# Kernel optimization log

Hardware: AMD Instinct MI355X
Metric: run time of the kernel (lower is better)

Reference implementation:

```python
import jax, jax.numpy as jnp
import numpy as np

B, N, D, H, L = 2, 2048, 128, 8, 3
V = 32          # NUM_ATOM_TYPES (assumed)
DH = D // H
SCALE = 1.0 / (DH ** 0.5)
NEG = -1e9      # stands in for -inf in the additive attention mask
EPS = 1e-5


def _ln(x, g, b):
    m = x.mean(-1, keepdims=True)
    v = ((x - m) ** 2).mean(-1, keepdims=True)
    return (x - m) / jnp.sqrt(v + EPS) * g + b


def setup_inputs() -> dict:
    key = jax.random.key(0)
    ks = jax.random.split(key, 24)
    nrm = lambda k, shape, std=0.02: jax.random.normal(k, shape, jnp.float32) * std
    atom_embed = nrm(ks[0], (V, D)).at[0].set(0.0)  # padding_idx = 0
    cons_embed = nrm(ks[1], (1, 1, D))
    in_w = nrm(ks[2], (D, D)); in_b = jnp.zeros((D,), jnp.float32)
    qkv_w = nrm(ks[3], (L, 3 * D, D)); qkv_b = jnp.zeros((L, 3 * D), jnp.float32)
    out_w = nrm(ks[4], (L, D, D)); out_b = jnp.zeros((L, D), jnp.float32)
    ln1_g = jnp.ones((L, D), jnp.float32); ln1_b = jnp.zeros((L, D), jnp.float32)
    ln2_g = jnp.ones((L, D), jnp.float32); ln2_b = jnp.zeros((L, D), jnp.float32)
    ff1_w = nrm(ks[5], (L, 4 * D, D)); ff1_b = jnp.zeros((L, 4 * D), jnp.float32)
    ff2_w = nrm(ks[6], (L, D, 4 * D)); ff2_b = jnp.zeros((L, D), jnp.float32)
    struct_bias = nrm(ks[7], (L,), 0.5)  # scalar per layer (init 0 in torch; randomized to exercise the path)
    head_ln_g = jnp.ones((D,), jnp.float32); head_ln_b = jnp.zeros((D,), jnp.float32)
    head_w = nrm(ks[8], (1, D)); head_b = jnp.zeros((1,), jnp.float32)
    is_atom = jax.random.bernoulli(ks[9], 0.5, (B, N))
    atom_id = jax.random.randint(ks[10], (B, N), 0, V)
    mask = jax.random.bernoulli(ks[11], 0.9, (B, N))
    adjacency = (jax.random.uniform(ks[12], (B, N, N)) < 0.002).astype(jnp.float32)
    adjacency = jnp.maximum(adjacency, jnp.eye(N, dtype=jnp.float32)[None])  # self-loops
    root_idx = jax.random.randint(ks[13], (B,), 0, N)
    return dict(atom_embed=atom_embed, cons_embed=cons_embed, in_w=in_w, in_b=in_b,
                qkv_w=qkv_w, qkv_b=qkv_b, out_w=out_w, out_b=out_b,
                ln1_g=ln1_g, ln1_b=ln1_b, ln2_g=ln2_g, ln2_b=ln2_b,
                ff1_w=ff1_w, ff1_b=ff1_b, ff2_w=ff2_w, ff2_b=ff2_b,
                struct_bias=struct_bias, head_ln_g=head_ln_g, head_ln_b=head_ln_b,
                head_w=head_w, head_b=head_b, adjacency=adjacency,
                is_atom=is_atom, atom_id=atom_id, mask=mask, root_idx=root_idx)


def reference(atom_embed, cons_embed, in_w, in_b, qkv_w, qkv_b, out_w, out_b,
              ln1_g, ln1_b, ln2_g, ln2_b, ff1_w, ff1_b, ff2_w, ff2_b,
              struct_bias, head_ln_g, head_ln_b, head_w, head_b,
              adjacency, is_atom, atom_id, mask, root_idx):
    # node embeddings
    ae = atom_embed[jnp.clip(atom_id, 0, V - 1)]                     # [B,N,D]
    h = jnp.where(is_atom[..., None], ae, jnp.broadcast_to(cons_embed, (B, N, D)))
    h = h @ in_w.T + in_b
    # additive attention mask: valid pairs OK; invalid query rows attend only to self
    pair_ok = mask[:, :, None] & mask[:, None, :]
    eye = jnp.eye(N, dtype=bool)[None]
    ok = pair_ok | ((~mask)[:, :, None] & eye)
    am = jnp.where(ok, 0.0, NEG).astype(jnp.float32)                 # [B,N,N]
    for i in range(L):
        x = _ln(h, ln1_g[i], ln1_b[i])
        qkv = (x @ qkv_w[i].T + qkv_b[i]).reshape(B, N, 3, H, DH)
        q, k, v = (jnp.transpose(qkv[:, :, j], (0, 2, 1, 3)) for j in range(3))  # [B,H,N,DH]
        scores = jnp.einsum('bhqd,bhkd->bhqk', q, k) * SCALE \
                 + struct_bias[i] * adjacency[:, None] + am[:, None]
        attn = jax.nn.softmax(scores, axis=-1)
        o = jnp.einsum('bhqk,bhkd->bhqd', attn, v)
        o = jnp.transpose(o, (0, 2, 1, 3)).reshape(B, N, D)
        h = h + (o @ out_w[i].T + out_b[i])
        x2 = _ln(h, ln2_g[i], ln2_b[i])
        f = jax.nn.gelu(x2 @ ff1_w[i].T + ff1_b[i], approximate=False)
        h = h + (f @ ff2_w[i].T + ff2_b[i])
    pooled = h[jnp.arange(B), root_idx]                              # [B,D]
    p = _ln(pooled, head_ln_g, head_ln_b)
    return (p @ head_w.T + head_b)[:, 0]                             # [B]
```

## Files before the change

kernel.cpp:

```cpp
#include <hip/hip_runtime.h>
#include <cmath>

#define NB 2
#define NN 2048
#define ND 128
#define NH 8
#define NL 3
#define NV 32
#define NDH 16
#define LN_EPS 1e-5f
#define QSCALE 0.36067376022224085f

typedef __bf16 bf8_t __attribute__((ext_vector_type(8)));
typedef __bf16 bf4_t __attribute__((ext_vector_type(4)));
typedef float f4x __attribute__((ext_vector_type(4)));
typedef float f16x __attribute__((ext_vector_type(16)));

struct CastArgs {
  const float* s[5];
  __bf16* d[5];
  int startblk[5];
};
__global__ __launch_bounds__(256) void prep_kernel(
    CastArgs a, const float* __restrict__ adj, unsigned long long* __restrict__ abits,
    const int* __restrict__ mask, unsigned long long* __restrict__ mbits) {
  int blk = blockIdx.x;
  int lane = threadIdx.x & 63;
  if (blk < 592) {
    int seg = 0;
#pragma unroll
    for (int i = 1; i < 5; i++) seg += (blk >= a.startblk[i]) ? 1 : 0;
    int i4 = (blk - a.startblk[seg]) * 256 + threadIdx.x;
    float4 v = ((const float4*)a.s[seg])[i4];
    bf4_t p = {(__bf16)v.x, (__bf16)v.y, (__bf16)v.z, (__bf16)v.w};
    ((bf4_t*)a.d[seg])[i4] = p;
  } else if (blk < 592 + 8192) {
    int g = ((blk - 592) * 4 + (threadIdx.x >> 6)) * 4;
    const float* p = adj + (size_t)g * 64 + lane;
    unsigned long long w0 = __ballot(p[0] != 0.0f);
    unsigned long long w1 = __ballot(p[64] != 0.0f);
    unsigned long long w2 = __ballot(p[128] != 0.0f);
    unsigned long long w3 = __ballot(p[192] != 0.0f);
    if (lane == 0) {
      abits[g] = w0; abits[g + 1] = w1; abits[g + 2] = w2; abits[g + 3] = w3;
    }
  } else {
    int g = (blk - 8784) * 4 + (threadIdx.x >> 6);
    int v = mask[g * 64 + lane];
    unsigned long long bal = __ballot(v != 0);
    if (lane == 0) mbits[g] = bal;
  }
}

__global__ __launch_bounds__(512) void fused0_kernel(
    const float* __restrict__ atom_embed, const float* __restrict__ cons_embed,
    const int* __restrict__ is_atom, const int* __restrict__ atom_id,
    const __bf16* __restrict__ W1, const float* __restrict__ b1,
    float* __restrict__ Hout,
    const float* __restrict__ lng, const float* __restrict__ lnb,
    const __bf16* __restrict__ W2, const float* __restrict__ b2,
    __bf16* __restrict__ Qb, __bf16* __restrict__ Kb, __bf16* __restrict__ Vt) {
  __shared__ __bf16 Xs[16][136];
  __shared__ __bf16 Ws[128][136];
  __shared__ float Hs[16][132];
  __shared__ __bf16 X2[16][136];
  int m0 = blockIdx.x * 16;
  int g = blockIdx.y;
  int t = threadIdx.x;
  int lane = t & 63, w = t >> 6;
  int l15 = lane & 15, quad = lane >> 4;
  const int NC2 = (g == 0) ? 2 : 1;
  const int T = 1 + NC2;

  {
    int r = t >> 5, c = t & 31;
    int row = m0 + r;
    int id = atom_id[row];
    id = id < 0 ? 0 : (id > NV - 1 ? NV - 1 : id);
    const float* src = is_atom[row] ? (atom_embed + (size_t)id * ND) : cons_embed;
    float4 v = *(const float4*)&src[c * 4];
    bf4_t p = {(__bf16)v.x, (__bf16)v.y, (__bf16)v.z, (__bf16)v.w};
    *(bf4_t*)&Xs[r][c * 4] = p;
  }

  bf8_t wreg[4];
  auto issue = [&](int i) {
    const __bf16* base;
    int rowoff;
    if (i == 0) { base = W1; rowoff = 0; }
    else {
      int nc = (g == 0) ? (i - 1) : 2;
      base = W2; rowoff = nc * 128;
    }
#pragma unroll
    for (int jj = 0; jj < 4; jj++) {
      int c = t + jj * 512;
      wreg[jj] = *(const bf8_t*)&base[(size_t)(rowoff + (c >> 4)) * 128 + (c & 15) * 8];
    }
  };
  issue(0);

  for (int i = 0; i < T; i++) {
    if (i) __syncthreads();
#pragma unroll
    for (int jj = 0; jj < 4; jj++) {
      int c = t + jj * 512;
      *(bf8_t*)&Ws[c >> 4][(c & 15) * 8] = wreg[jj];
    }
    __syncthreads();
    if (i + 1 < T) issue(i + 1);
    if (i == 0) {
      f4x a1 = {0.f, 0.f, 0.f, 0.f};
#pragma unroll
      for (int kk = 0; kk < 4; kk++) {
        bf8_t a = *(const bf8_t*)&Xs[l15][kk * 32 + quad * 8];
        bf8_t b = *(const bf8_t*)&Ws[w * 16 + l15][kk * 32 + quad * 8];
        a1 = __builtin_amdgcn_mfma_f32_16x16x32_bf16(a, b, a1, 0, 0, 0);
      }
      int n = w * 16 + l15;
      float bv = b1[n];
#pragma unroll
      for (int r = 0; r < 4; r++) {
        int m = quad * 4 + r;
        float v = a1[r] + bv;
        if (g == 0) Hout[(size_t)(m0 + m) * ND + n] = v;
        Hs[m][n] = v;
      }
      __syncthreads();
      {
        int r = t >> 5, c = t & 31;
        float4 v = *(const float4*)&Hs[r][c * 4];
        float s1 = v.x + v.y + v.z + v.w;
        float s2 = v.x * v.x + v.y * v.y + v.z * v.z + v.w * v.w;
#pragma unroll
        for (int m = 16; m >= 1; m >>= 1) {
          s1 += __shfl_xor(s1, m, 64);
          s2 += __shfl_xor(s2, m, 64);
        }
        float mean = s1 * (1.0f / ND);
        float var = s2 * (1.0f / ND) - mean * mean;
        float rstd = rsqrtf(var + LN_EPS);
        float4 gg = *(const float4*)&lng[c * 4];
        float4 bb = *(const float4*)&lnb[c * 4];
        bf4_t p;
        p[0] = (__bf16)((v.x - mean) * rstd * gg.x + bb.x);
        p[1] = (__bf16)((v.y - mean) * rstd * gg.y + bb.y);
        p[2] = (__bf16)((v.z - mean) * rstd * gg.z + bb.z);
        p[3] = (__bf16)((v.w - mean) * rstd * gg.w + bb.w);
        *(bf4_t*)&X2[r][c * 4] = p;
      }
    } else {
      int nc = (g == 0) ? (i - 1) : 2;
      f4x a2 = {0.f, 0.f, 0.f, 0.f};
#pragma unroll
      for (int kk = 0; kk < 4; kk++) {
        bf8_t a = *(const bf8_t*)&X2[l15][kk * 32 + quad * 8];
        bf8_t b = *(const bf8_t*)&Ws[w * 16 + l15][kk * 32 + quad * 8];
        a2 = __builtin_amdgcn_mfma_f32_16x16x32_bf16(a, b, a2, 0, 0, 0);
      }
      int n = nc * 128 + w * 16 + l15;
      float bv = b2[n];
#pragma unroll
      for (int r = 0; r < 4; r++) {
        int m = m0 + quad * 4 + r;
        float v = a2[r] + bv;
        if (n < ND) Qb[(size_t)m * ND + n] = (__bf16)(v * QSCALE);
        else if (n < 2 * ND) Kb[(size_t)m * ND + n - ND] = (__bf16)v;
        else {
          int c2 = n - 2 * ND, hh = c2 >> 4, d0 = c2 & 15;
          int bb2 = m >> 11, nn = m & 2047;
          Vt[((size_t)((bb2 * NH + hh) * NDH + d0)) * NN + nn] = (__bf16)v;
        }
      }
    }
  }
}

template <int LAST>
__global__ __launch_bounds__(512) void layer_kernel(
    const __bf16* __restrict__ Ob,
    const __bf16* __restrict__ Wout, const float* __restrict__ bout,
    const float* __restrict__ Hin, float* __restrict__ Hout,
    const float* __restrict__ ln2g, const float* __restrict__ ln2b,
    const __bf16* __restrict__ Wff1, const float* __restrict__ bff1,
    const __bf16* __restrict__ Wff2, const float* __restrict__ bff2,
    const float* __restrict__ ln1g, const float* __restrict__ ln1b,
    const __bf16* __restrict__ Wqkv, const float* __restrict__ bqkv,
    __bf16* __restrict__ Qb, __bf16* __restrict__ Kb, __bf16* __restrict__ Vt,
    const int* __restrict__ root_idx, const float* __restrict__ hg,
    const float* __restrict__ hbt, const float* __restrict__ hwp,
    const float* __restrict__ hbp, float* __restrict__ outp) {
  __shared__ __bf16 Xs[16][136];
  __shared__ __bf16 Ws[128][136];
  __shared__ float Hs[16][132];
  __shared__ __bf16 X2[16][136];
  __shared__ __bf16 Fs[16][520];
  int m0 = blockIdx.x * 16;
  int g = blockIdx.y;
  int t = threadIdx.x;
  int lane = t & 63, w = t >> 6;
  int l15 = lane & 15, quad = lane >> 4;
  const int NQ = LAST ? 0 : (g == 0 ? 2 : 1);
  const int T = 9 + NQ;

  {
    int r = t >> 5, c = t & 31;
    *(bf4_t*)&Xs[r][c * 4] = *(const bf4_t*)&Ob[(size_t)(m0 + r) * ND + c * 4];
  }

  bf8_t wreg[4];
  auto issue = [&](int i) {
    const __bf16* base;
    int stride, rowoff, coloff;
    if (i == 0)     { base = Wout; stride = 128; rowoff = 0;             coloff = 0; }
    else if (i < 5) { base = Wff1; stride = 128; rowoff = (i - 1) * 128; coloff = 0; }
    else if (i < 9) { base = Wff2; stride = 512; rowoff = 0;             coloff = (i - 5) * 128; }
    else            { int nc = (g == 0) ? (i - 9) : 2;
                      base = Wqkv; stride = 128; rowoff = nc * 128;      coloff = 0; }
#pragma unroll
    for (int jj = 0; jj < 4; jj++) {
      int c = t + jj * 512;
      wreg[jj] = *(const bf8_t*)&base[(size_t)(rowoff + (c >> 4)) * stride + coloff + (c & 15) * 8];
    }
  };
  issue(0);

  auto do_ln = [&](const float* g_, const float* b_) {
    int r = t >> 5, c = t & 31;
    float4 v = *(const float4*)&Hs[r][c * 4];
    float s1 = v.x + v.y + v.z + v.w;
    float s2 = v.x * v.x + v.y * v.y + v.z * v.z + v.w * v.w;
#pragma unroll
    for (int m = 16; m >= 1; m >>= 1) {
      s1 += __shfl_xor(s1, m, 64);
      s2 += __shfl_xor(s2, m, 64);
    }
    float mean = s1 * (1.0f / ND);
    float var = s2 * (1.0f / ND) - mean * mean;
    float rstd = rsqrtf(var + LN_EPS);
    float4 gg = *(const float4*)&g_[c * 4];
    float4 bb = *(const float4*)&b_[c * 4];
    bf4_t p;
    p[0] = (__bf16)((v.x - mean) * rstd * gg.x + bb.x);
    p[1] = (__bf16)((v.y - mean) * rstd * gg.y + bb.y);
    p[2] = (__bf16)((v.z - mean) * rstd * gg.z + bb.z);
    p[3] = (__bf16)((v.w - mean) * rstd * gg.w + bb.w);
    *(bf4_t*)&X2[r][c * 4] = p;
  };

  f4x acc2 = {0.f, 0.f, 0.f, 0.f};
  for (int i = 0; i < T; i++) {
    if (i) __syncthreads();
#pragma unroll
    for (int jj = 0; jj < 4; jj++) {
      int c = t + jj * 512;
      *(bf8_t*)&Ws[c >> 4][(c & 15) * 8] = wreg[jj];
    }
    __syncthreads();
    if (i + 1 < T) issue(i + 1);
    if (i == 0) {
      f4x a1 = {0.f, 0.f, 0.f, 0.f};
#pragma unroll
      for (int kk = 0; kk < 4; kk++) {
        bf8_t a = *(const bf8_t*)&Xs[l15][kk * 32 + quad * 8];
        bf8_t b = *(const bf8_t*)&Ws[w * 16 + l15][kk * 32 + quad * 8];
        a1 = __builtin_amdgcn_mfma_f32_16x16x32_bf16(a, b, a1, 0, 0, 0);
      }
      int n = w * 16 + l15;
      float bv = bout[n];
#pragma unroll
      for (int r = 0; r < 4; r++) {
        int m = quad * 4 + r;
        Hs[m][n] = a1[r] + bv + Hin[(size_t)(m0 + m) * ND + n];
      }
      __syncthreads();
      do_ln(ln2g, ln2b);
    } else if (i < 5) {
      int c = i - 1;
      f4x a1 = {0.f, 0.f, 0.f, 0.f};
#pragma unroll
      for (int kk = 0; kk < 4; kk++) {
        bf8_t a = *(const bf8_t*)&X2[l15][kk * 32 + quad * 8];
        bf8_t b = *(const bf8_t*)&Ws[w * 16 + l15][kk * 32 + quad * 8];
        a1 = __builtin_amdgcn_mfma_f32_16x16x32_bf16(a, b, a1, 0, 0, 0);
      }
      int n = w * 16 + l15;
      float bv = bff1[c * 128 + n];
#pragma unroll
      for (int r = 0; r < 4; r++) {
        float v = a1[r] + bv;
        v = 0.5f * v * (1.0f + erff(v * 0.70710678118f));
        Fs[quad * 4 + r][c * 128 + n] = (__bf16)v;
      }
    } else if (i < 9) {
      int j = i - 5;
#pragma unroll
      for (int kk = 0; kk < 4; kk++) {
        bf8_t a = *(const bf8_t*)&Fs[l15][j * 128 + kk * 32 + quad * 8];
        bf8_t b = *(const bf8_t*)&Ws[w * 16 + l15][kk * 32 + quad * 8];
        acc2 = __builtin_amdgcn_mfma_f32_16x16x32_bf16(a, b, acc2, 0, 0, 0);
      }
      if (j == 3) {
        int n = w * 16 + l15;
        float bv = bff2[n];
#pragma unroll
        for (int r = 0; r < 4; r++) {
          int m = quad * 4 + r;
          float v = acc2[r] + bv + Hs[m][n];
          Hs[m][n] = v;
          if (g == 0) Hout[(size_t)(m0 + m) * ND + n] = v;
        }
        __syncthreads();
        if constexpr (!LAST) do_ln(ln1g, ln1b);
      }
    } else {
      int nc = (g == 0) ? (i - 9) : 2;
      f4x a2 = {0.f, 0.f, 0.f, 0.f};
#pragma unroll
      for (int kk = 0; kk < 4; kk++) {
        bf8_t a = *(const bf8_t*)&X2[l15][kk * 32 + quad * 8];
        bf8_t b = *(const bf8_t*)&Ws[w * 16 + l15][kk * 32 + quad * 8];
        a2 = __builtin_amdgcn_mfma_f32_16x16x32_bf16(a, b, a2, 0, 0, 0);
      }
      int n = nc * 128 + w * 16 + l15;
      float bv = bqkv[n];
#pragma unroll
      for (int r = 0; r < 4; r++) {
        int m = m0 + quad * 4 + r;
        float v = a2[r] + bv;
        if (n < ND) Qb[(size_t)m * ND + n] = (__bf16)(v * QSCALE);
        else if (n < 2 * ND) Kb[(size_t)m * ND + n - ND] = (__bf16)v;
        else {
          int c2 = n - 2 * ND, hh = c2 >> 4, d0 = c2 & 15;
          int bb2 = m >> 11, nn = m & 2047;
          Vt[((size_t)((bb2 * NH + hh) * NDH + d0)) * NN + nn] = (__bf16)v;
        }
      }
    }
  }

  if constexpr (LAST) {
    if (w < NB) {
      int rt = root_idx[w];
      int rglob = w * NN + rt;
      if (rglob >= m0 && rglob < m0 + 16) {
        int r = rglob - m0;
        float v0 = Hs[r][2 * lane], v1 = Hs[r][2 * lane + 1];
        float s1 = v0 + v1, s2 = v0 * v0 + v1 * v1;
#pragma unroll
        for (int m = 32; m >= 1; m >>= 1) {
          s1 += __shfl_xor(s1, m, 64);
          s2 += __shfl_xor(s2, m, 64);
        }
        float mean = s1 * (1.0f / ND);
        float var = s2 * (1.0f / ND) - mean * mean;
        float rstd = rsqrtf(var + LN_EPS);
        float p0 = (v0 - mean) * rstd * hg[2 * lane] + hbt[2 * lane];
        float p1 = (v1 - mean) * rstd * hg[2 * lane + 1] + hbt[2 * lane + 1];
        float part = p0 * hwp[2 * lane] + p1 * hwp[2 * lane + 1];
#pragma unroll
        for (int m = 32; m >= 1; m >>= 1) part += __shfl_xor(part, m, 64);
        if (lane == 0) outp[w] = part + hbp[0];
      }
    }
  }
}

__global__ __launch_bounds__(512) void attn_kernel(
    const __bf16* __restrict__ Qb, const __bf16* __restrict__ Kb,
    const __bf16* __restrict__ Vt, const unsigned int* __restrict__ adjbits,
    const unsigned int* __restrict__ maskbits, const int* __restrict__ mask,
    const float* __restrict__ sbias, int layer, __bf16* __restrict__ o) {
  int b = blockIdx.z, hh = blockIdx.y, q0 = blockIdx.x * 32;
  int wave = threadIdx.x >> 6;
  int lane = threadIdx.x & 63;
  int l31 = lane & 31, hi = lane >> 5;
  int l15 = lane & 15, quad = lane >> 4;
  float esb = __expf(sbias[layer]);
  const int bN = b * NN;
  const int kw0 = wave * 256;

  __shared__ __bf16 Pbuf[8][32][40];
  __shared__ float Ored[8][32][17];
  __shared__ float Lred[8][32];

  bf8_t Qf = *(const bf8_t*)(Qb + (size_t)(bN + q0 + l31) * ND + hh * NDH + hi * 8);

  int q = q0 + l31;
  int mq = mask[bN + q];
  const unsigned int* adjp = adjbits + (size_t)(bN + q) * (NN / 32) + (kw0 >> 5);
  const unsigned int* mbp = maskbits + (bN + kw0) / 32;
  const __bf16* kp = Kb + (size_t)(bN + kw0 + l31) * ND + hh * NDH + hi * 8;
  const __bf16* vp = Vt + (size_t)((b * NH + hh) * NDH + l15) * NN + kw0 + quad * 8;

  int dq = q - kw0;
  int tsel = dq >> 5;
  unsigned int selfw = 1u << (dq & 31);
  int sh4 = hi * 4;

  f4x Olo = {0.f, 0.f, 0.f, 0.f}, Ohi = {0.f, 0.f, 0.f, 0.f};
  float ls = 0.f;

  bf8_t Kf = *(const bf8_t*)kp;
  bf8_t Vf = *(const bf8_t*)vp;
  unsigned int aw = adjp[0];
  unsigned int mkw = mbp[0];

  for (int t = 0; t < 8; t++) {
    bf8_t Kn = Kf, Vn = Vf;
    unsigned int awn = aw, mkn = mkw;
    if (t < 7) {
      kp += 32 * ND;
      Kn = *(const bf8_t*)kp;
      Vn = *(const bf8_t*)(vp + (t + 1) * 32);
      awn = adjp[t + 1];
      mkn = mbp[t + 1];
    }
    f16x S = {0.f, 0.f, 0.f, 0.f, 0.f, 0.f, 0.f, 0.f,
              0.f, 0.f, 0.f, 0.f, 0.f, 0.f, 0.f, 0.f};
    S = __builtin_amdgcn_mfma_f32_32x32x16_bf16(Kf, Qf, S, 0, 0, 0);
    unsigned int okw = mq ? mkw : ((t == tsel) ? selfw : 0u);
    unsigned int wa = (aw & okw) >> sh4;
    unsigned int okh = okw >> sh4;
#pragma unroll
    for (int gg = 0; gg < 4; gg++) {
      bf4_t pk;
#pragma unroll
      for (int r = 0; r < 4; r++) {
        int c = gg * 8 + r;
        float e = __builtin_amdgcn_exp2f(S[gg * 4 + r]);
        float wgt = ((wa >> c) & 1) ? esb : (((okh >> c) & 1) ? 1.0f : 0.0f);
        float p = e * wgt;
        ls += p;
        pk[r] = (__bf16)p;
      }
      *(bf4_t*)&Pbuf[wave][l31][sh4 + gg * 8] = pk;
    }
    asm volatile("s_waitcnt lgkmcnt(0)" ::: "memory");
    bf8_t Plo = *(const bf8_t*)&Pbuf[wave][l15][quad * 8];
    bf8_t Phi = *(const bf8_t*)&Pbuf[wave][16 + l15][quad * 8];
    Olo = __builtin_amdgcn_mfma_f32_16x16x32_bf16(Plo, Vf, Olo, 0, 0, 0);
    Ohi = __builtin_amdgcn_mfma_f32_16x16x32_bf16(Phi, Vf, Ohi, 0, 0, 0);
    Kf = Kn; Vf = Vn; aw = awn; mkw = mkn;
  }

  ls += __shfl_xor(ls, 32, 64);
  if (hi == 0) Lred[wave][l31] = ls;
#pragma unroll
  for (int r = 0; r < 4; r++) {
    Ored[wave][quad * 4 + r][l15] = Olo[r];
    Ored[wave][16 + quad * 4 + r][l15] = Ohi[r];
  }
  __syncthreads();
  int row = threadIdx.x >> 4, col = threadIdx.x & 15;
  float s = 0.f, L = 0.f;
#pragma unroll
  for (int p = 0; p < 8; p++) {
    s += Ored[p][row][col];
    L += Lred[p][row];
  }
  o[(size_t)(bN + q0 + row) * ND + hh * NDH + col] = (__bf16)(s / L);
}

extern "C" void kernel_launch(void* const* d_in, const int* in_sizes, int n_in,
                              void* d_out, int out_size, void* d_ws, size_t ws_size,
                              hipStream_t stream) {
  const float* atom_embed = (const float*)d_in[0];
  const float* cons_embed = (const float*)d_in[1];
  const float* in_w  = (const float*)d_in[2];
  const float* in_b  = (const float*)d_in[3];
  const float* qkv_w = (const float*)d_in[4];
  const float* qkv_b = (const float*)d_in[5];
  const float* out_w = (const float*)d_in[6];
  const float* out_b = (const float*)d_in[7];
  const float* ln1_g = (const float*)d_in[8];
  const float* ln1_b = (const float*)d_in[9];
  const float* ln2_g = (const float*)d_in[10];
  const float* ln2_b = (const float*)d_in[11];
  const float* ff1_w = (const float*)d_in[12];
  const float* ff1_b = (const float*)d_in[13];
  const float* ff2_w = (const float*)d_in[14];
  const float* ff2_b = (const float*)d_in[15];
  const float* sbias = (const float*)d_in[16];
  const float* hg    = (const float*)d_in[17];
  const float* hbt   = (const float*)d_in[18];
  const float* hw    = (const float*)d_in[19];
  const float* hb    = (const float*)d_in[20];
  const float* adj   = (const float*)d_in[21];
  const int* is_atom = (const int*)d_in[22];
  const int* atom_id = (const int*)d_in[23];
  const int* mask    = (const int*)d_in[24];
  const int* root_idx= (const int*)d_in[25];
  float* out = (float*)d_out;

  const int MR = NB * NN;
  float* hA = (float*)d_ws;
  float* hB = hA + MR * ND;
  __bf16* Qb   = (__bf16*)(hB + MR * ND);
  __bf16* Kb   = Qb + MR * ND;
  __bf16* Vt   = Kb + MR * ND;
  __bf16* wbin = Vt + MR * ND;
  __bf16* wbqkv= wbin + ND * ND;
  __bf16* wbout= wbqkv + NL * 384 * ND;
  __bf16* wbff1= wbout + NL * ND * ND;
  __bf16* wbff2= wbff1 + NL * 512 * ND;
  unsigned int* adjb = (unsigned int*)(wbff2 + NL * ND * 512);
  unsigned int* mskb = adjb + NB * NN * NN / 32;
  __bf16* ob = (__bf16*)(mskb + 128);

  CastArgs ca;
  ca.s[0] = in_w;  ca.d[0] = wbin;  ca.startblk[0] = 0;
  ca.s[1] = qkv_w; ca.d[1] = wbqkv; ca.startblk[1] = 16;
  ca.s[2] = out_w; ca.d[2] = wbout; ca.startblk[2] = 160;
  ca.s[3] = ff1_w; ca.d[3] = wbff1; ca.startblk[3] = 208;
  ca.s[4] = ff2_w; ca.d[4] = wbff2; ca.startblk[4] = 400;
  prep_kernel<<<8800, 256, 0, stream>>>(ca, adj, (unsigned long long*)adjb,
                                        mask, (unsigned long long*)mskb);

  fused0_kernel<<<dim3(MR / 16, 2), 512, 0, stream>>>(
      atom_embed, cons_embed, is_atom, atom_id,
      wbin, in_b, hA, ln1_g, ln1_b, wbqkv, qkv_b, Qb, Kb, Vt);

  const float* hin[3]  = {hA, hB, hA};
  float* hout[3]       = {hB, hA, hB};
  for (int i = 0; i < NL; i++) {
    attn_kernel<<<dim3(NN / 32, NH, NB), 512, 0, stream>>>(
        Qb, Kb, Vt, adjb, mskb, mask, sbias, i, ob);
    if (i < NL - 1) {
      layer_kernel<0><<<dim3(MR / 16, 2), 512, 0, stream>>>(
          ob, wbout + (size_t)i * ND * ND, out_b + i * ND, hin[i], hout[i],
          ln2_g + i * ND, ln2_b + i * ND,
          wbff1 + (size_t)i * 512 * ND, ff1_b + i * 512,
          wbff2 + (size_t)i * ND * 512, ff2_b + i * ND,
          ln1_g + (i + 1) * ND, ln1_b + (i + 1) * ND,
          wbqkv + (size_t)(i + 1) * 384 * ND, qkv_b + (i + 1) * 384,
          Qb, Kb, Vt,
          nullptr, nullptr, nullptr, nullptr, nullptr, nullptr);
    } else {
      layer_kernel<1><<<dim3(MR / 16, 1), 512, 0, stream>>>(
          ob, wbout + (size_t)i * ND * ND, out_b + i * ND, hin[i], hout[i],
          ln2_g + i * ND, ln2_b + i * ND,
          wbff1 + (size_t)i * 512 * ND, ff1_b + i * 512,
          wbff2 + (size_t)i * ND * 512, ff2_b + i * ND,
          nullptr, nullptr, nullptr, nullptr,
          nullptr, nullptr, nullptr,
          root_idx, hg, hbt, hw, hb, out);
    }
  }
}
```

Baseline: 259.9 us.

## Load MFMA weight fragments directly into registers and drop split-grid QKV blocks

Weight tiles are no longer staged through a shared-memory buffer with block-wide barriers. Each lane now loads its MFMA B-operand fragments straight from global memory into registers, double-buffered one stage ahead. The second grid dimension, which split the QKV projection across two block groups (recomputing the whole prefix in each), is removed so one block does all QKV chunks. This cuts LDS traffic, barriers and duplicated work, but each block now runs more stages serially with fewer blocks in flight, and global loads are less coalesced.

```diff
diff --git a/kernel.cpp b/kernel.cpp
--- a/kernel.cpp
+++ b/kernel.cpp
@@ -61,16 +61,13 @@
     const __bf16* __restrict__ W2, const float* __restrict__ b2,
     __bf16* __restrict__ Qb, __bf16* __restrict__ Kb, __bf16* __restrict__ Vt) {
   __shared__ __bf16 Xs[16][136];
-  __shared__ __bf16 Ws[128][136];
   __shared__ float Hs[16][132];
   __shared__ __bf16 X2[16][136];
   int m0 = blockIdx.x * 16;
-  int g = blockIdx.y;
   int t = threadIdx.x;
   int lane = t & 63, w = t >> 6;
   int l15 = lane & 15, quad = lane >> 4;
-  const int NC2 = (g == 0) ? 2 : 1;
-  const int T = 1 + NC2;
+  int wrow = w * 16 + l15;
 
   {
     int r = t >> 5, c = t & 31;
@@ -83,47 +80,32 @@
     *(bf4_t*)&Xs[r][c * 4] = p;
   }
 
-  bf8_t wreg[4];
-  auto issue = [&](int i) {
-    const __bf16* base;
-    int rowoff;
-    if (i == 0) { base = W1; rowoff = 0; }
-    else {
-      int nc = (g == 0) ? (i - 1) : 2;
-      base = W2; rowoff = nc * 128;
-    }
-#pragma unroll
-    for (int jj = 0; jj < 4; jj++) {
-      int c = t + jj * 512;
-      wreg[jj] = *(const bf8_t*)&base[(size_t)(rowoff + (c >> 4)) * 128 + (c & 15) * 8];
-    }
+  bf8_t wcur[4], wnxt[4];
+  auto issue = [&](int i, bf8_t* dst) {
+    const __bf16* base = (i == 0) ? W1 : (W2 + (size_t)(i - 1) * 128 * 128);
+    const __bf16* p = base + (size_t)wrow * 128 + quad * 8;
+#pragma unroll
+    for (int kk = 0; kk < 4; kk++) dst[kk] = *(const bf8_t*)(p + kk * 32);
   };
-  issue(0);
-
-  for (int i = 0; i < T; i++) {
-    if (i) __syncthreads();
-#pragma unroll
-    for (int jj = 0; jj < 4; jj++) {
-      int c = t + jj * 512;
-      *(bf8_t*)&Ws[c >> 4][(c & 15) * 8] = wreg[jj];
-    }
-    __syncthreads();
-    if (i + 1 < T) issue(i + 1);
+  issue(0, wcur);
+  __syncthreads();
+
+  for (int i = 0; i < 4; i++) {
+    if (i + 1 < 4) issue(i + 1, wnxt);
     if (i == 0) {
       f4x a1 = {0.f, 0.f, 0.f, 0.f};
 #pragma unroll
       for (int kk = 0; kk < 4; kk++) {
         bf8_t a = *(const bf8_t*)&Xs[l15][kk * 32 + quad * 8];
-        bf8_t b = *(const bf8_t*)&Ws[w * 16 + l15][kk * 32 + quad * 8];
-        a1 = __builtin_amdgcn_mfma_f32_16x16x32_bf16(a, b, a1, 0, 0, 0);
-      }
-      int n = w * 16 + l15;
+        a1 = __builtin_amdgcn_mfma_f32_16x16x32_bf16(a, wcur[kk], a1, 0, 0, 0);
+      }
+      int n = wrow;
       float bv = b1[n];
 #pragma unroll
       for (int r = 0; r < 4; r++) {
         int m = quad * 4 + r;
         float v = a1[r] + bv;
-        if (g == 0) Hout[(size_t)(m0 + m) * ND + n] = v;
+        Hout[(size_t)(m0 + m) * ND + n] = v;
         Hs[m][n] = v;
       }
       __syncthreads();
@@ -149,16 +131,16 @@
         p[3] = (__bf16)((v.w - mean) * rstd * gg.w + bb.w);
         *(bf4_t*)&X2[r][c * 4] = p;
       }
+      __syncthreads();
     } else {
-      int nc = (g == 0) ? (i - 1) : 2;
+      int nc = i - 1;
       f4x a2 = {0.f, 0.f, 0.f, 0.f};
 #pragma unroll
       for (int kk = 0; kk < 4; kk++) {
         bf8_t a = *(const bf8_t*)&X2[l15][kk * 32 + quad * 8];
-        bf8_t b = *(const bf8_t*)&Ws[w * 16 + l15][kk * 32 + quad * 8];
-        a2 = __builtin_amdgcn_mfma_f32_16x16x32_bf16(a, b, a2, 0, 0, 0);
-      }
-      int n = nc * 128 + w * 16 + l15;
+        a2 = __builtin_amdgcn_mfma_f32_16x16x32_bf16(a, wcur[kk], a2, 0, 0, 0);
+      }
+      int n = nc * 128 + wrow;
       float bv = b2[n];
 #pragma unroll
       for (int r = 0; r < 4; r++) {
@@ -173,6 +155,8 @@
         }
       }
     }
+#pragma unroll
+    for (int kk = 0; kk < 4; kk++) wcur[kk] = wnxt[kk];
   }
 }
 
@@ -191,39 +175,33 @@
     const float* __restrict__ hbt, const float* __restrict__ hwp,
     const float* __restrict__ hbp, float* __restrict__ outp) {
   __shared__ __bf16 Xs[16][136];
-  __shared__ __bf16 Ws[128][136];
   __shared__ float Hs[16][132];
   __shared__ __bf16 X2[16][136];
   __shared__ __bf16 Fs[16][520];
   int m0 = blockIdx.x * 16;
-  int g = blockIdx.y;
   int t = threadIdx.x;
   int lane = t & 63, w = t >> 6;
   int l15 = lane & 15, quad = lane >> 4;
-  const int NQ = LAST ? 0 : (g == 0 ? 2 : 1);
-  const int T = 9 + NQ;
+  int wrow = w * 16 + l15;
+  const int T = LAST ? 9 : 12;
 
   {
     int r = t >> 5, c = t & 31;
     *(bf4_t*)&Xs[r][c * 4] = *(const bf4_t*)&Ob[(size_t)(m0 + r) * ND + c * 4];
   }
 
-  bf8_t wreg[4];
-  auto issue = [&](int i) {
-    const __bf16* base;
-    int stride, rowoff, coloff;
-    if (i == 0)     { base = Wout; stride = 128; rowoff = 0;             coloff = 0; }
-    else if (i < 5) { base = Wff1; stride = 128; rowoff = (i - 1) * 128; coloff = 0; }
-    else if (i < 9) { base = Wff2; stride = 512; rowoff = 0;             coloff = (i - 5) * 128; }
-    else            { int nc = (g == 0) ? (i - 9) : 2;
-                      base = Wqkv; stride = 128; rowoff = nc * 128;      coloff = 0; }
-#pragma unroll
-    for (int jj = 0; jj < 4; jj++) {
-      int c = t + jj * 512;
-      wreg[jj] = *(const bf8_t*)&base[(size_t)(rowoff + (c >> 4)) * stride + coloff + (c & 15) * 8];
-    }
+  bf8_t wcur[4], wnxt[4];
+  auto issue = [&](int i, bf8_t* dst) {
+    const __bf16* p;
+    if (i == 0)     p = Wout + (size_t)wrow * 128 + quad * 8;
+    else if (i < 5) p = Wff1 + ((size_t)((i - 1) * 128 + wrow)) * 128 + quad * 8;
+    else if (i < 9) p = Wff2 + (size_t)wrow * 512 + (i - 5) * 128 + quad * 8;
+    else            p = Wqkv + ((size_t)((i - 9) * 128 + wrow)) * 128 + quad * 8;
+#pragma unroll
+    for (int kk = 0; kk < 4; kk++) dst[kk] = *(const bf8_t*)(p + kk * 32);
   };
-  issue(0);
+  issue(0, wcur);
+  __syncthreads();
 
   auto do_ln = [&](const float* g_, const float* b_) {
     int r = t >> 5, c = t & 31;
@@ -250,23 +228,15 @@
 
   f4x acc2 = {0.f, 0.f, 0.f, 0.f};
   for (int i = 0; i < T; i++) {
-    if (i) __syncthreads();
-#pragma unroll
-    for (int jj = 0; jj < 4; jj++) {
-      int c = t + jj * 512;
-      *(bf8_t*)&Ws[c >> 4][(c & 15) * 8] = wreg[jj];
-    }
-    __syncthreads();
-    if (i + 1 < T) issue(i + 1);
+    if (i + 1 < T) issue(i + 1, wnxt);
     if (i == 0) {
       f4x a1 = {0.f, 0.f, 0.f, 0.f};
 #pragma unroll
       for (int kk = 0; kk < 4; kk++) {
         bf8_t a = *(const bf8_t*)&Xs[l15][kk * 32 + quad * 8];
-        bf8_t b = *(const bf8_t*)&Ws[w * 16 + l15][kk * 32 + quad * 8];
-        a1 = __builtin_amdgcn_mfma_f32_16x16x32_bf16(a, b, a1, 0, 0, 0);
-      }
-      int n = w * 16 + l15;
+        a1 = __builtin_amdgcn_mfma_f32_16x16x32_bf16(a, wcur[kk], a1, 0, 0, 0);
+      }
+      int n = wrow;
       float bv = bout[n];
 #pragma unroll
       for (int r = 0; r < 4; r++) {
@@ -275,16 +245,16 @@
       }
       __syncthreads();
       do_ln(ln2g, ln2b);
+      __syncthreads();
     } else if (i < 5) {
       int c = i - 1;
       f4x a1 = {0.f, 0.f, 0.f, 0.f};
 #pragma unroll
       for (int kk = 0; kk < 4; kk++) {
         bf8_t a = *(const bf8_t*)&X2[l15][kk * 32 + quad * 8];
-        bf8_t b = *(const bf8_t*)&Ws[w * 16 + l15][kk * 32 + quad * 8];
-        a1 = __builtin_amdgcn_mfma_f32_16x16x32_bf16(a, b, a1, 0, 0, 0);
-      }
-      int n = w * 16 + l15;
+        a1 = __builtin_amdgcn_mfma_f32_16x16x32_bf16(a, wcur[kk], a1, 0, 0, 0);
+      }
+      int n = wrow;
       float bv = bff1[c * 128 + n];
 #pragma unroll
       for (int r = 0; r < 4; r++) {
@@ -292,37 +262,39 @@
         v = 0.5f * v * (1.0f + erff(v * 0.70710678118f));
         Fs[quad * 4 + r][c * 128 + n] = (__bf16)v;
       }
+      if (i == 4) __syncthreads();
     } else if (i < 9) {
       int j = i - 5;
 #pragma unroll
       for (int kk = 0; kk < 4; kk++) {
         bf8_t a = *(const bf8_t*)&Fs[l15][j * 128 + kk * 32 + quad * 8];
-        bf8_t b = *(const bf8_t*)&Ws[w * 16 + l15][kk * 32 + quad * 8];
-        acc2 = __builtin_amdgcn_mfma_f32_16x16x32_bf16(a, b, acc2, 0, 0, 0);
+        acc2 = __builtin_amdgcn_mfma_f32_16x16x32_bf16(a, wcur[kk], acc2, 0, 0, 0);
       }
       if (j == 3) {
-        int n = w * 16 + l15;
+        int n = wrow;
         float bv = bff2[n];
 #pragma unroll
         for (int r = 0; r < 4; r++) {
           int m = quad * 4 + r;
           float v = acc2[r] + bv + Hs[m][n];
           Hs[m][n] = v;
-          if (g == 0) Hout[(size_t)(m0 + m) * ND + n] = v;
+          Hout[(size_t)(m0 + m) * ND + n] = v;
         }
         __syncthreads();
-        if constexpr (!LAST) do_ln(ln1g, ln1b);
+        if constexpr (!LAST) {
+          do_ln(ln1g, ln1b);
+          __syncthreads();
+        }
       }
     } else {
-      int nc = (g == 0) ? (i - 9) : 2;
+      int nc = i - 9;
       f4x a2 = {0.f, 0.f, 0.f, 0.f};
 #pragma unroll
       for (int kk = 0; kk < 4; kk++) {
         bf8_t a = *(const bf8_t*)&X2[l15][kk * 32 + quad * 8];
-        bf8_t b = *(const bf8_t*)&Ws[w * 16 + l15][kk * 32 + quad * 8];
-        a2 = __builtin_amdgcn_mfma_f32_16x16x32_bf16(a, b, a2, 0, 0, 0);
-      }
-      int n = nc * 128 + w * 16 + l15;
+        a2 = __builtin_amdgcn_mfma_f32_16x16x32_bf16(a, wcur[kk], a2, 0, 0, 0);
+      }
+      int n = nc * 128 + wrow;
       float bv = bqkv[n];
 #pragma unroll
       for (int r = 0; r < 4; r++) {
@@ -337,6 +309,8 @@
         }
       }
     }
+#pragma unroll
+    for (int kk = 0; kk < 4; kk++) wcur[kk] = wnxt[kk];
   }
 
   if constexpr (LAST) {
@@ -517,7 +491,7 @@
   prep_kernel<<<8800, 256, 0, stream>>>(ca, adj, (unsigned long long*)adjb,
                                         mask, (unsigned long long*)mskb);
 
-  fused0_kernel<<<dim3(MR / 16, 2), 512, 0, stream>>>(
+  fused0_kernel<<<dim3(MR / 16), 512, 0, stream>>>(
       atom_embed, cons_embed, is_atom, atom_id,
       wbin, in_b, hA, ln1_g, ln1_b, wbqkv, qkv_b, Qb, Kb, Vt);
 
@@ -527,7 +501,7 @@
     attn_kernel<<<dim3(NN / 32, NH, NB), 512, 0, stream>>>(
         Qb, Kb, Vt, adjb, mskb, mask, sbias, i, ob);
     if (i < NL - 1) {
-      layer_kernel<0><<<dim3(MR / 16, 2), 512, 0, stream>>>(
+      layer_kernel<0><<<dim3(MR / 16), 512, 0, stream>>>(
           ob, wbout + (size_t)i * ND * ND, out_b + i * ND, hin[i], hout[i],
           ln2_g + i * ND, ln2_b + i * ND,
           wbff1 + (size_t)i * 512 * ND, ff1_b + i * 512,
@@ -537,7 +511,7 @@
           Qb, Kb, Vt,
           nullptr, nullptr, nullptr, nullptr, nullptr, nullptr);
     } else {
-      layer_kernel<1><<<dim3(MR / 16, 1), 512, 0, stream>>>(
+      layer_kernel<1><<<dim3(MR / 16), 512, 0, stream>>>(
           ob, wbout + (size_t)i * ND * ND, out_b + i * ND, hin[i], hout[i],
           ln2_g + i * ND, ln2_b + i * ND,
           wbff1 + (size_t)i * 512 * ND, ff1_b + i * 512,
```

Result: no change. 259.6 us (-0.1%).
